# Kernel optimization log

Hardware: AMD Instinct MI355X
Metric: run time of the kernel (lower is better)

Reference implementation:

```python
import jax, jax.numpy as jnp
import numpy as np

N = 32768       # total nodes across the batch of graphs
E = 524288      # total edges
D = 512         # feature dim (dimensions = [512, 512, 512])
G = 512         # number of graphs (64 nodes each)


def setup_inputs() -> dict:
    key = jax.random.key(0)
    ks = jax.random.split(key, 16)
    inp = {
        'feat': jax.random.normal(ks[0], (N, D), jnp.float32),
        'src': jax.random.randint(ks[1], (E,), 0, N, jnp.int32),
        'dst': jax.random.randint(ks[2], (E,), 0, N, jnp.int32),
        'adj_vals': jax.random.uniform(ks[3], (E,), jnp.float32),
        'graph_ids': (jnp.arange(N, dtype=jnp.int32) // (N // G)),
        'W0': jax.random.normal(ks[4], (D, D), jnp.float32) * 0.05,
        'b0': jnp.zeros((D,), jnp.float32),
        'W1': jax.random.normal(ks[5], (D, D), jnp.float32) * 0.05,
        'b1': jnp.zeros((D,), jnp.float32),
        'gW1': jax.random.normal(ks[6], (D, D), jnp.float32) * 0.05,
        'gb1': jnp.zeros((D,), jnp.float32),
        'gW2': jax.random.normal(ks[7], (D, D), jnp.float32) * 0.05,
        'gb2': jnp.zeros((D,), jnp.float32),
        'gW3': jax.random.normal(ks[8], (D, D), jnp.float32) * 0.05,
        'gb3': jnp.zeros((D,), jnp.float32),
        'gWs': jax.random.normal(ks[9], (D, D), jnp.float32) * 0.05,
        'gbs': jnp.zeros((D,), jnp.float32),
    }
    return inp


def reference(feat, src, dst, adj_vals, graph_ids,
              W0, b0, W1, b1,
              gW1, gb1, gW2, gb2, gW3, gb3, gWs, gbs):
    # GCN layer: act(A_hat @ (X W) + b), A_hat given as weighted edge list
    def gcn(h, W, b, act):
        support = h @ W                              # [N, D]
        msg = adj_vals[:, None] * support[src]       # [E, D]
        agg = jax.ops.segment_sum(msg, dst, num_segments=N)
        return act(agg + b)

    h = gcn(feat, W0, b0, jax.nn.relu)               # hidden layer, act=relu
    h = gcn(h, W1, b1, lambda x: x)                  # last layer, identity act

    # pooling: per-graph mean readout -> sigmoid -> repeat-expand back to nodes
    ones = jnp.ones((N, 1), h.dtype)
    counts = jax.ops.segment_sum(ones, graph_ids, num_segments=G)   # [G, 1]
    pooled = jax.ops.segment_sum(h, graph_ids, num_segments=G) / counts
    g = jax.nn.sigmoid(pooled)[graph_ids]            # [N, D] repeat-expanded

    z = jax.nn.relu(g @ gW1 + gb1)
    z = jax.nn.relu(z @ gW2 + gb2)
    z = jax.nn.relu(z @ gW3 + gb3)
    return z + (g @ gWs + gbs)
```

## Files before the change

### kernel.cpp

```cpp
#include <hip/hip_runtime.h>

typedef unsigned int u32;
typedef unsigned short u16;

typedef __attribute__((ext_vector_type(8))) __bf16 bf16x8;
typedef __attribute__((ext_vector_type(4))) float f32x4;
typedef __attribute__((ext_vector_type(2))) float f32x2;
typedef __attribute__((ext_vector_type(4))) u32 u32x4;

#define N_NODES 32768
#define N_EDGES 524288
#define DIM 512
#define N_GRAPHS 512
#define ECAP_ROW 768
#define ECAP 1216
#define ELDS_SZ (ECAP + ECAP / 32 + 1)
#define NB_CONV 8192
#define NB_TR 1536

__device__ __forceinline__ u16 f2b(float f) {
  union { float f; u32 u; } v; v.f = f;
  u32 r = v.u + 0x7FFFu + ((v.u >> 16) & 1u);
  return (u16)(r >> 16);
}
__device__ __forceinline__ u32 pack2(float a, float b) {
  return (u32)f2b(a) | ((u32)f2b(b) << 16);
}
__device__ __forceinline__ float blo(u32 u) { union { u32 u; float f; } v; v.u = u << 16; return v.f; }
__device__ __forceinline__ float bhi(u32 u) { union { u32 u; float f; } v; v.u = u & 0xFFFF0000u; return v.f; }
__device__ __forceinline__ float b2f(u16 u) { union { u32 u; float f; } v; v.u = ((u32)u) << 16; return v.f; }

__device__ __forceinline__ void async16(const void* g, void* l) {
  __builtin_amdgcn_global_load_lds(
      (const __attribute__((address_space(1))) u32*)g,
      (__attribute__((address_space(3))) u32*)l, 16, 0, 0);
}

__device__ __forceinline__ int eidx(int i) { return i + (i >> 5); }

__device__ __forceinline__ void acc8(f32x2* a, u32x4 raw, float v) {
  f32x2 v2 = {v, v};
  a[0] += v2 * f32x2{blo(raw.x), bhi(raw.x)};
  a[1] += v2 * f32x2{blo(raw.y), bhi(raw.y)};
  a[2] += v2 * f32x2{blo(raw.z), bhi(raw.z)};
  a[3] += v2 * f32x2{blo(raw.w), bhi(raw.w)};
}

struct WPack {
  const float* src[6];
  u16* dst[6];
};
__global__ __launch_bounds__(256)
void k_prep(const float* __restrict__ feat, u16* __restrict__ featb, WPack wp,
            const int* __restrict__ dstv, int* __restrict__ counts) {
  __shared__ float tile[32][33];
  const int bid = blockIdx.x, tid = threadIdx.x;
  if (bid < NB_CONV) {
    int i = bid * 256 + tid;
    const float4* p = (const float4*)feat;
    float4 a = p[2 * i], b = p[2 * i + 1];
    uint4 o;
    o.x = pack2(a.x, a.y); o.y = pack2(a.z, a.w);
    o.z = pack2(b.x, b.y); o.w = pack2(b.z, b.w);
    ((uint4*)featb)[i] = o;
  } else if (bid < NB_CONV + NB_TR) {
    int idx = bid - NB_CONV;
    int bz = idx >> 8, rem = idx & 255, by = rem >> 4, bx = rem & 15;
    const float* W = wp.src[bz];
    u16* Wt = wp.dst[bz];
    int tx = tid & 31, ty = tid >> 5;
    int bx32 = bx * 32, by32 = by * 32;
    #pragma unroll
    for (int i = 0; i < 4; i++)
      tile[ty + 8 * i][tx] = W[(size_t)(by32 + ty + 8 * i) * DIM + bx32 + tx];
    __syncthreads();
    #pragma unroll
    for (int i = 0; i < 4; i++)
      Wt[(size_t)(bx32 + ty + 8 * i) * DIM + by32 + tx] = f2b(tile[tx][ty + 8 * i]);
  } else {
    int i = (bid - NB_CONV - NB_TR) * 256 + tid;
    atomicAdd(&counts[dstv[i]], 1);
  }
}

__global__ void k_scan(const int* __restrict__ counts, int* __restrict__ offsets,
                       int* __restrict__ cursor) {
  __shared__ int part[1024];
  int t = threadIdx.x;
  const int4* c4 = (const int4*)counts;
  int4 cv[8];
  #pragma unroll
  for (int j = 0; j < 8; j++) cv[j] = c4[t * 8 + j];
  int loc[32];
  int s = 0;
  #pragma unroll
  for (int j = 0; j < 8; j++) {
    loc[4 * j + 0] = s; s += cv[j].x;
    loc[4 * j + 1] = s; s += cv[j].y;
    loc[4 * j + 2] = s; s += cv[j].z;
    loc[4 * j + 3] = s; s += cv[j].w;
  }
  part[t] = s;
  __syncthreads();
  for (int off = 1; off < 1024; off <<= 1) {
    int v = (t >= off) ? part[t - off] : 0;
    __syncthreads();
    part[t] += v;
    __syncthreads();
  }
  int excl = (t == 0) ? 0 : part[t - 1];
  #pragma unroll
  for (int j = 0; j < 8; j++) {
    int4 o = make_int4(excl + loc[4 * j], excl + loc[4 * j + 1],
                       excl + loc[4 * j + 2], excl + loc[4 * j + 3]);
    ((int4*)offsets)[t * 8 + j] = o;
    ((int4*)cursor)[t * 8 + j] = o;
  }
  if (t == 1023) offsets[N_NODES] = excl + s;
}

__global__ void k_fill(const int* __restrict__ src, const int* __restrict__ dst,
                       const float* __restrict__ vals, int* __restrict__ cursor,
                       int2* __restrict__ epack) {
  int i = blockIdx.x * 256 + threadIdx.x;
  if (i >= N_EDGES) return;
  int d = dst[i];
  int p = atomicAdd(&cursor[d], 1);
  epack[p] = make_int2(src[i] | ((d & 63) << 15), __float_as_int(vals[i]));
}

__global__ __launch_bounds__(256)
void k_gemm_bt(const u16* __restrict__ A, const u16* __restrict__ Bt,
               u16* __restrict__ Cout, int M, int Nout, int K) {
  __shared__ __align__(16) u16 As[128 * 32];
  __shared__ __align__(16) u16 Bs[128 * 32];
  const int tid = threadIdx.x;
  const int l = tid & 63;
  const int w = tid >> 6;
  const int mBase = blockIdx.x * 128;
  const int nBase = blockIdx.y * 128;
  const int wm = (w >> 1) * 64;
  const int wn = (w & 1) * 64;
  const int lrow = l >> 2;
  const int lcol = (l & 3) * 8;
  const int q = l >> 4;
  const int r = l & 15;
  f32x4 acc[4][4] = {};

  for (int k0 = 0; k0 < K; k0 += 32) {
    #pragma unroll
    for (int p = 0; p < 2; p++) {
      int row = w * 32 + p * 16 + lrow;
      async16(A + (size_t)(mBase + row) * K + k0 + lcol, (char*)As + w * 2048 + p * 1024);
      async16(Bt + (size_t)(nBase + row) * K + k0 + lcol, (char*)Bs + w * 2048 + p * 1024);
    }
    __syncthreads();
    bf16x8 af[4], bfr[4];
    #pragma unroll
    for (int i = 0; i < 4; i++) af[i] = *(const bf16x8*)&As[(wm + i * 16 + r) * 32 + q * 8];
    #pragma unroll
    for (int j = 0; j < 4; j++) bfr[j] = *(const bf16x8*)&Bs[(wn + j * 16 + r) * 32 + q * 8];
    #pragma unroll
    for (int i = 0; i < 4; i++)
      #pragma unroll
      for (int j = 0; j < 4; j++)
        acc[i][j] = __builtin_amdgcn_mfma_f32_16x16x32_bf16(af[i], bfr[j], acc[i][j], 0, 0, 0);
    __syncthreads();
  }

  #pragma unroll
  for (int i = 0; i < 4; i++) {
    #pragma unroll
    for (int j = 0; j < 4; j++) {
      int col = nBase + wn + j * 16 + r;
      #pragma unroll
      for (int reg = 0; reg < 4; reg++) {
        int rowg = mBase + wm + i * 16 + q * 4 + reg;
        Cout[(size_t)rowg * Nout + col] = f2b(acc[i][j][reg]);
      }
    }
  }
}

template <bool RELU, bool ADDEND, bool OUTF32, bool SIGMOID>
__global__ __launch_bounds__(256)
void k_gemm_small(const u16* __restrict__ A, const u16* __restrict__ Bt,
                  const float* __restrict__ bias, const u16* __restrict__ addend,
                  void* __restrict__ Cout) {
  constexpr int K = 512, Nout = 512, LDP = 520;
  __shared__ __align__(16) u16 As[64 * LDP];
  __shared__ __align__(16) u16 Bs[64 * LDP];
  const int tid = threadIdx.x;
  const int l = tid & 63;
  const int w = tid >> 6;
  const int mBase = blockIdx.x * 64;
  const int nBase = blockIdx.y * 64;
  const int wm = (w >> 1) * 32;
  const int wn = (w & 1) * 32;
  const int q = l >> 4;
  const int r = l & 15;

  {
    const int row0 = tid >> 6;
    const int c8 = (tid & 63) * 8;
    #pragma unroll
    for (int s = 0; s < 16; s++) {
      int row = s * 4 + row0;
      *(bf16x8*)&As[row * LDP + c8] = *(const bf16x8*)&A[(size_t)(mBase + row) * K + c8];
      *(bf16x8*)&Bs[row * LDP + c8] = *(const bf16x8*)&Bt[(size_t)(nBase + row) * K + c8];
    }
  }
  __syncthreads();

  f32x4 acc[2][2] = {};
  #pragma unroll
  for (int k = 0; k < 16; k++) {
    bf16x8 af0 = *(const bf16x8*)&As[(wm + r) * LDP + k * 32 + q * 8];
    bf16x8 af1 = *(const bf16x8*)&As[(wm + 16 + r) * LDP + k * 32 + q * 8];
    bf16x8 bf0 = *(const bf16x8*)&Bs[(wn + r) * LDP + k * 32 + q * 8];
    bf16x8 bf1 = *(const bf16x8*)&Bs[(wn + 16 + r) * LDP + k * 32 + q * 8];
    acc[0][0] = __builtin_amdgcn_mfma_f32_16x16x32_bf16(af0, bf0, acc[0][0], 0, 0, 0);
    acc[0][1] = __builtin_amdgcn_mfma_f32_16x16x32_bf16(af0, bf1, acc[0][1], 0, 0, 0);
    acc[1][0] = __builtin_amdgcn_mfma_f32_16x16x32_bf16(af1, bf0, acc[1][0], 0, 0, 0);
    acc[1][1] = __builtin_amdgcn_mfma_f32_16x16x32_bf16(af1, bf1, acc[1][1], 0, 0, 0);
  }

  #pragma unroll
  for (int i = 0; i < 2; i++) {
    #pragma unroll
    for (int j = 0; j < 2; j++) {
      int col = nBase + wn + j * 16 + r;
      float bv = bias[col];
      #pragma unroll
      for (int reg = 0; reg < 4; reg++) {
        int rowg = mBase + wm + i * 16 + q * 4 + reg;
        float v = acc[i][j][reg] + bv;
        if (ADDEND) v += b2f(addend[(size_t)rowg * Nout + col]);
        if (RELU) v = fmaxf(v, 0.0f);
        if (SIGMOID) v = 1.0f / (1.0f + expf(-v));
        if (OUTF32) ((float*)Cout)[(size_t)rowg * Nout + col] = v;
        else ((u16*)Cout)[(size_t)rowg * Nout + col] = f2b(v);
      }
    }
  }
}

__global__ __launch_bounds__(256)
void k_agg_row(const u16* __restrict__ support, const int* __restrict__ offsets,
               const int2* __restrict__ epack, const float* __restrict__ bias,
               u16* __restrict__ outp) {
  __shared__ int2 eLds[ECAP_ROW];
  __shared__ unsigned char permLds[32];
  const int tid = threadIdx.x;
  const int chunk = blockIdx.x & 7;
  const int gidx  = blockIdx.x >> 3;
  const int rowBase = gidx * 32;
  const int e0b = offsets[rowBase];
  const int nb = offsets[rowBase + 32] - e0b;
  const bool fits = (nb <= ECAP_ROW);

  if (tid < 32) {
    int deg = offsets[rowBase + tid + 1] - offsets[rowBase + tid];
    u32 key = ((u32)deg << 8) | (u32)tid;
    #pragma unroll
    for (int k = 2; k <= 32; k <<= 1) {
      #pragma unroll
      for (int j = k >> 1; j >= 1; j >>= 1) {
        u32 o = __shfl_xor(key, j);
        bool lower = (tid & j) == 0;
        bool asc = (tid & k) == 0;
        key = ((key < o) == (lower == asc)) ? key : o;
      }
    }
    permLds[tid] = (unsigned char)(key & 255u);
  }
  if (fits) {
    for (int i = tid; i < nb; i += 256) eLds[i] = epack[e0b + i];
  }
  __syncthreads();

  const int wi = tid >> 6;
  const int l  = tid & 63;
  const int grp = l >> 3;
  const int li  = l & 7;
  const int colOff = chunk * 64 + li * 8;
  const u16* spc = support + colOff;

  const int rl = permLds[wi * 8 + grp];
  const int r = rowBase + rl;
  const int re0 = offsets[r] - e0b;
  const int deg = offsets[r + 1] - e0b - re0;

  f32x2 a[4];
  {
    const float4* bp = (const float4*)(bias + colOff);
    float4 x = bp[0], y = bp[1];
    a[0] = f32x2{x.x, x.y}; a[1] = f32x2{x.z, x.w};
    a[2] = f32x2{y.x, y.y}; a[3] = f32x2{y.z, y.w};
  }

  if (fits) {
    int i = 0;
    for (; i + 8 <= deg; i += 8) {
      int2 p[8];
      #pragma unroll
      for (int j = 0; j < 8; j++) p[j] = eLds[re0 + i + j];
      u32x4 rw[8];
      #pragma unroll
      for (int j = 0; j < 8; j++)
        rw[j] = *(const u32x4*)(spc + (size_t)(p[j].x & 32767) * DIM);
      #pragma unroll
      for (int j = 0; j < 8; j++) acc8(a, rw[j], __int_as_float(p[j].y));
    }
    for (; i < deg; i++) {
      int2 p = eLds[re0 + i];
      u32x4 rw = *(const u32x4*)(spc + (size_t)(p.x & 32767) * DIM);
      acc8(a, rw, __int_as_float(p.y));
    }
  } else {
    for (int i = 0; i < deg; i++) {
      int2 p = epack[e0b + re0 + i];
      u32x4 rw = *(const u32x4*)(spc + (size_t)(p.x & 32767) * DIM);
      acc8(a, rw, __int_as_float(p.y));
    }
  }

  #pragma unroll
  for (int i = 0; i < 4; i++) {
    a[i].x = fmaxf(a[i].x, 0.0f);
    a[i].y = fmaxf(a[i].y, 0.0f);
  }
  u32x4 o;
  o.x = pack2(a[0].x, a[0].y); o.y = pack2(a[1].x, a[1].y);
  o.z = pack2(a[2].x, a[2].y); o.w = pack2(a[3].x, a[3].y);
  *(u32x4*)(outp + (size_t)r * DIM + colOff) = o;
}

__global__ __launch_bounds__(256)
void k_agg_pool(const u16* __restrict__ support, const int* __restrict__ offsets,
                const int2* __restrict__ epack, u16* __restrict__ outp) {
  __shared__ int2 eLds[ELDS_SZ];
  __shared__ float redLds[256];

  const int tid = threadIdx.x;
  const int chunk = blockIdx.x & 7;
  const int cidx = blockIdx.x >> 3;
  const int rowBase = cidx * 64;
  const int e0b = offsets[rowBase];
  const int nb = offsets[rowBase + 64] - e0b;
  const bool fits = (nb <= ECAP);

  if (fits) {
    for (int i = tid; i < nb; i += 256) eLds[eidx(i)] = epack[e0b + i];
  }
  __syncthreads();

  const int slot = tid >> 3;
  const int li = tid & 7;
  const int colOff = chunk * 64 + li * 8;
  const u16* spc = support + colOff;
  const int e0 = (nb * slot) >> 5;
  const int e1 = (nb * (slot + 1)) >> 5;

  f32x2 psum[4] = {};

  auto consume = [&](int2 p, u32x4 rw) {
    float v = __int_as_float(p.y);
    f32x2 v2 = {v, v};
    psum[0] += v2 * f32x2{blo(rw.x), bhi(rw.x)};
    psum[1] += v2 * f32x2{blo(rw.y), bhi(rw.y)};
    psum[2] += v2 * f32x2{blo(rw.z), bhi(rw.z)};
    psum[3] += v2 * f32x2{blo(rw.w), bhi(rw.w)};
  };

  if (fits) {
    int i = e0;
    for (; i + 8 <= e1; i += 8) {
      int2 p[8];
      #pragma unroll
      for (int j = 0; j < 8; j++) p[j] = eLds[eidx(i + j)];
      u32x4 rw[8];
      #pragma unroll
      for (int j = 0; j < 8; j++)
        rw[j] = *(const u32x4*)(spc + (size_t)(p[j].x & 32767) * DIM);
      #pragma unroll
      for (int j = 0; j < 8; j++) consume(p[j], rw[j]);
    }
    for (; i < e1; i++) {
      int2 p = eLds[eidx(i)];
      u32x4 rw = *(const u32x4*)(spc + (size_t)(p.x & 32767) * DIM);
      consume(p, rw);
    }
  } else {
    for (int i = e0; i < e1; i++) {
      int2 p = epack[e0b + i];
      u32x4 rw = *(const u32x4*)(spc + (size_t)(p.x & 32767) * DIM);
      consume(p, rw);
    }
  }

  #pragma unroll
  for (int k = 0; k < 4; k++) {
    psum[k].x += __shfl_xor(psum[k].x, 8);  psum[k].y += __shfl_xor(psum[k].y, 8);
    psum[k].x += __shfl_xor(psum[k].x, 16); psum[k].y += __shfl_xor(psum[k].y, 16);
    psum[k].x += __shfl_xor(psum[k].x, 32); psum[k].y += __shfl_xor(psum[k].y, 32);
  }
  const int wi = tid >> 6;
  if (((tid >> 3) & 7) == 0) {
    #pragma unroll
    for (int k = 0; k < 4; k++) {
      redLds[wi * 64 + li * 8 + 2 * k]     = psum[k].x;
      redLds[wi * 64 + li * 8 + 2 * k + 1] = psum[k].y;
    }
  }
  __syncthreads();
  if (tid < 64) {
    float s = redLds[tid] + redLds[64 + tid] + redLds[128 + tid] + redLds[192 + tid];
    outp[(size_t)cidx * DIM + chunk * 64 + tid] = f2b(s * (1.0f / 64.0f));
  }
}

__global__ void k_expand(const float* __restrict__ small, float* __restrict__ out) {
  int i = blockIdx.x * 256 + threadIdx.x;
  int col4 = i & 127;
  int node = i >> 7;
  float4 v = ((const float4*)small)[((node >> 6) << 7) + col4];
  ((float4*)out)[i] = v;
}

extern "C" void kernel_launch(void* const* d_in, const int* in_sizes, int n_in,
                              void* d_out, int out_size, void* d_ws, size_t ws_size,
                              hipStream_t stream) {
  const float* feat = (const float*)d_in[0];
  const int* src    = (const int*)d_in[1];
  const int* dst    = (const int*)d_in[2];
  const float* adj  = (const float*)d_in[3];
  const float* W0  = (const float*)d_in[5];
  const float* b0  = (const float*)d_in[6];
  const float* W1  = (const float*)d_in[7];
  const float* b1  = (const float*)d_in[8];
  const float* gW1 = (const float*)d_in[9];
  const float* gb1 = (const float*)d_in[10];
  const float* gW2 = (const float*)d_in[11];
  const float* gb2 = (const float*)d_in[12];
  const float* gW3 = (const float*)d_in[13];
  const float* gb3 = (const float*)d_in[14];
  const float* gWs = (const float*)d_in[15];
  const float* gbs = (const float*)d_in[16];

  char* ws = (char*)d_ws;
  size_t off = 0;
  auto alloc = [&](size_t bytes) -> void* {
    void* p = ws + off;
    off = (off + bytes + 255) & ~(size_t)255;
    return p;
  };
  u16* bufA = (u16*)alloc((size_t)N_NODES * DIM * 2);
  u16* bufB = (u16*)alloc((size_t)N_NODES * DIM * 2);
  u16* wt[6];
  for (int i = 0; i < 6; i++) wt[i] = (u16*)alloc((size_t)DIM * DIM * 2);
  int* counts   = (int*)alloc((size_t)N_NODES * 4);
  int* offsets  = (int*)alloc((size_t)(N_NODES + 1) * 4);
  int* cursor   = (int*)alloc((size_t)N_NODES * 4);
  int2* epack   = (int2*)alloc((size_t)N_EDGES * 8);
  u16* qb       = (u16*)alloc((size_t)N_GRAPHS * DIM * 2);
  u16* gfeat    = (u16*)alloc((size_t)N_GRAPHS * DIM * 2);
  u16* z1       = (u16*)alloc((size_t)N_GRAPHS * DIM * 2);
  u16* z2       = (u16*)alloc((size_t)N_GRAPHS * DIM * 2);
  u16* z3       = (u16*)alloc((size_t)N_GRAPHS * DIM * 2);
  float* osmall = (float*)alloc((size_t)N_GRAPHS * DIM * 4);

  (void)hipMemsetAsync(counts, 0, (size_t)N_NODES * 4, stream);

  WPack wp;
  wp.src[0] = W0; wp.src[1] = W1; wp.src[2] = gW1; wp.src[3] = gW2; wp.src[4] = gW3; wp.src[5] = gWs;
  for (int i = 0; i < 6; i++) wp.dst[i] = wt[i];

  k_prep<<<NB_CONV + NB_TR + N_EDGES / 256, 256, 0, stream>>>(feat, bufA, wp, dst, counts);
  k_scan<<<1, 1024, 0, stream>>>(counts, offsets, cursor);
  k_fill<<<N_EDGES / 256, 256, 0, stream>>>(src, dst, adj, cursor, epack);

  k_gemm_bt<<<dim3(N_NODES / 128, DIM / 128), 256, 0, stream>>>(bufA, wt[0], bufB, N_NODES, DIM, DIM);
  k_agg_row<<<8192, 256, 0, stream>>>(bufB, offsets, epack, b0, bufA);
  k_agg_pool<<<4096, 256, 0, stream>>>(bufA, offsets, epack, qb);
  k_gemm_small<false, false, false, true><<<dim3(8, 8), 256, 0, stream>>>(qb, wt[1], b1, nullptr, gfeat);

  k_gemm_small<true, false, false, false><<<dim3(8, 8), 256, 0, stream>>>(gfeat, wt[2], gb1, nullptr, z1);
  k_gemm_small<true, false, false, false><<<dim3(8, 8), 256, 0, stream>>>(z1, wt[3], gb2, nullptr, z2);
  k_gemm_small<true, false, false, false><<<dim3(8, 8), 256, 0, stream>>>(z2, wt[4], gb3, nullptr, z3);
  k_gemm_small<false, true, true, false><<<dim3(8, 8), 256, 0, stream>>>(gfeat, wt[5], gbs, z3, osmall);

  k_expand<<<(N_NODES * DIM / 4) / 256, 256, 0, stream>>>(osmall, (float*)d_out);
}
```

Baseline: 371.6 us.

## Fuse edge fill into first GEMM and chain small FF GEMMs with grid barrier

Merges the edge-bucketing fill kernel into the first feature GEMM launch as extra blocks, so the two independent pieces of work run concurrently in one dispatch. It also replaces five back-to-back small GEMM launches with one persistent 64-block kernel that uses a software global barrier between stages. The goal is to cut launch overhead and tail idle time. The cost is reliance on all 64 blocks being co-resident for the spin barrier, plus barrier spin latency.

```diff
diff --git a/kernel.cpp b/kernel.cpp
--- a/kernel.cpp
+++ b/kernel.cpp
@@ -44,6 +44,18 @@
   a[1] += v2 * f32x2{blo(raw.y), bhi(raw.y)};
   a[2] += v2 * f32x2{blo(raw.z), bhi(raw.z)};
   a[3] += v2 * f32x2{blo(raw.w), bhi(raw.w)};
+}
+
+__device__ __forceinline__ void gbar(int* bar, int target) {
+  __syncthreads();
+  if (threadIdx.x == 0) {
+    __threadfence();
+    __hip_atomic_fetch_add(bar, 1, __ATOMIC_RELEASE, __HIP_MEMORY_SCOPE_AGENT);
+    while (__hip_atomic_load(bar, __ATOMIC_ACQUIRE, __HIP_MEMORY_SCOPE_AGENT) < target) {
+      __builtin_amdgcn_s_sleep(2);
+    }
+  }
+  __syncthreads();
 }
 
 struct WPack {
@@ -119,26 +131,27 @@
   if (t == 1023) offsets[N_NODES] = excl + s;
 }
 
-__global__ void k_fill(const int* __restrict__ src, const int* __restrict__ dst,
-                       const float* __restrict__ vals, int* __restrict__ cursor,
-                       int2* __restrict__ epack) {
-  int i = blockIdx.x * 256 + threadIdx.x;
-  if (i >= N_EDGES) return;
-  int d = dst[i];
-  int p = atomicAdd(&cursor[d], 1);
-  epack[p] = make_int2(src[i] | ((d & 63) << 15), __float_as_int(vals[i]));
-}
-
 __global__ __launch_bounds__(256)
-void k_gemm_bt(const u16* __restrict__ A, const u16* __restrict__ Bt,
-               u16* __restrict__ Cout, int M, int Nout, int K) {
+void k_fillgemm(const u16* __restrict__ A, const u16* __restrict__ Bt,
+                u16* __restrict__ Cout,
+                const int* __restrict__ src, const int* __restrict__ dst,
+                const float* __restrict__ vals, int* __restrict__ cursor,
+                int2* __restrict__ epack) {
   __shared__ __align__(16) u16 As[128 * 32];
   __shared__ __align__(16) u16 Bs[128 * 32];
+  if (blockIdx.x >= 1024) {
+    int i = (blockIdx.x - 1024) * 256 + threadIdx.x;
+    int d = dst[i];
+    int p = atomicAdd(&cursor[d], 1);
+    epack[p] = make_int2(src[i] | ((d & 63) << 15), __float_as_int(vals[i]));
+    return;
+  }
+  constexpr int K = DIM, Nout = DIM;
   const int tid = threadIdx.x;
   const int l = tid & 63;
   const int w = tid >> 6;
-  const int mBase = blockIdx.x * 128;
-  const int nBase = blockIdx.y * 128;
+  const int mBase = (blockIdx.x >> 2) * 128;
+  const int nBase = (blockIdx.x & 3) * 128;
   const int wm = (w >> 1) * 64;
   const int wn = (w & 1) * 64;
   const int lrow = l >> 2;
@@ -182,19 +195,15 @@
   }
 }
 
-template <bool RELU, bool ADDEND, bool OUTF32, bool SIGMOID>
-__global__ __launch_bounds__(256)
-void k_gemm_small(const u16* __restrict__ A, const u16* __restrict__ Bt,
-                  const float* __restrict__ bias, const u16* __restrict__ addend,
-                  void* __restrict__ Cout) {
+template <int MODE>
+__device__ __forceinline__ void ff_stage(u16* As, u16* Bs,
+    const u16* __restrict__ A, const u16* __restrict__ Bt,
+    const float* __restrict__ bias, const u16* __restrict__ addend,
+    void* __restrict__ Cout, int mBase, int nBase) {
   constexpr int K = 512, Nout = 512, LDP = 520;
-  __shared__ __align__(16) u16 As[64 * LDP];
-  __shared__ __align__(16) u16 Bs[64 * LDP];
   const int tid = threadIdx.x;
   const int l = tid & 63;
   const int w = tid >> 6;
-  const int mBase = blockIdx.x * 64;
-  const int nBase = blockIdx.y * 64;
   const int wm = (w >> 1) * 32;
   const int wn = (w & 1) * 32;
   const int q = l >> 4;
@@ -235,14 +244,40 @@
       for (int reg = 0; reg < 4; reg++) {
         int rowg = mBase + wm + i * 16 + q * 4 + reg;
         float v = acc[i][j][reg] + bv;
-        if (ADDEND) v += b2f(addend[(size_t)rowg * Nout + col]);
-        if (RELU) v = fmaxf(v, 0.0f);
-        if (SIGMOID) v = 1.0f / (1.0f + expf(-v));
-        if (OUTF32) ((float*)Cout)[(size_t)rowg * Nout + col] = v;
+        if (MODE == 2) v += b2f(addend[(size_t)rowg * Nout + col]);
+        if (MODE == 1) v = fmaxf(v, 0.0f);
+        if (MODE == 0) v = 1.0f / (1.0f + expf(-v));
+        if (MODE == 2) ((float*)Cout)[(size_t)rowg * Nout + col] = v;
         else ((u16*)Cout)[(size_t)rowg * Nout + col] = f2b(v);
       }
     }
   }
+}
+
+__global__ __launch_bounds__(256)
+void k_ffchain(const u16* __restrict__ qb,
+               const u16* __restrict__ w1, const float* __restrict__ b1v,
+               const u16* __restrict__ w2, const float* __restrict__ gb1,
+               const u16* __restrict__ w3, const float* __restrict__ gb2,
+               const u16* __restrict__ w4, const float* __restrict__ gb3,
+               const u16* __restrict__ w5, const float* __restrict__ gbs,
+               u16* __restrict__ gfeat, u16* __restrict__ z1,
+               u16* __restrict__ z2, u16* __restrict__ z3,
+               float* __restrict__ osmall, int* bar) {
+  __shared__ __align__(16) u16 As[64 * 520];
+  __shared__ __align__(16) u16 Bs[64 * 520];
+  const int mBase = (int)(blockIdx.x >> 3) * 64;
+  const int nBase = (int)(blockIdx.x & 7) * 64;
+
+  ff_stage<0>(As, Bs, qb,    w1, b1v, nullptr, gfeat, mBase, nBase);
+  gbar(bar, 64);
+  ff_stage<1>(As, Bs, gfeat, w2, gb1, nullptr, z1, mBase, nBase);
+  gbar(bar, 128);
+  ff_stage<1>(As, Bs, z1,    w3, gb2, nullptr, z2, mBase, nBase);
+  gbar(bar, 192);
+  ff_stage<1>(As, Bs, z2,    w4, gb3, nullptr, z3, mBase, nBase);
+  gbar(bar, 256);
+  ff_stage<2>(As, Bs, gfeat, w5, gbs, z3, osmall, mBase, nBase);
 }
 
 __global__ __launch_bounds__(256)
@@ -469,8 +504,10 @@
   u16* z2       = (u16*)alloc((size_t)N_GRAPHS * DIM * 2);
   u16* z3       = (u16*)alloc((size_t)N_GRAPHS * DIM * 2);
   float* osmall = (float*)alloc((size_t)N_GRAPHS * DIM * 4);
+  int* bar      = (int*)alloc(256);
 
   (void)hipMemsetAsync(counts, 0, (size_t)N_NODES * 4, stream);
+  (void)hipMemsetAsync(bar, 0, 4, stream);
 
   WPack wp;
   wp.src[0] = W0; wp.src[1] = W1; wp.src[2] = gW1; wp.src[3] = gW2; wp.src[4] = gW3; wp.src[5] = gWs;
@@ -478,17 +515,15 @@
 
   k_prep<<<NB_CONV + NB_TR + N_EDGES / 256, 256, 0, stream>>>(feat, bufA, wp, dst, counts);
   k_scan<<<1, 1024, 0, stream>>>(counts, offsets, cursor);
-  k_fill<<<N_EDGES / 256, 256, 0, stream>>>(src, dst, adj, cursor, epack);
-
-  k_gemm_bt<<<dim3(N_NODES / 128, DIM / 128), 256, 0, stream>>>(bufA, wt[0], bufB, N_NODES, DIM, DIM);
+
+  k_fillgemm<<<3072, 256, 0, stream>>>(bufA, wt[0], bufB, src, dst, adj, cursor, epack);
+
   k_agg_row<<<8192, 256, 0, stream>>>(bufB, offsets, epack, b0, bufA);
   k_agg_pool<<<4096, 256, 0, stream>>>(bufA, offsets, epack, qb);
-  k_gemm_small<false, false, false, true><<<dim3(8, 8), 256, 0, stream>>>(qb, wt[1], b1, nullptr, gfeat);
-
-  k_gemm_small<true, false, false, false><<<dim3(8, 8), 256, 0, stream>>>(gfeat, wt[2], gb1, nullptr, z1);
-  k_gemm_small<true, false, false, false><<<dim3(8, 8), 256, 0, stream>>>(z1, wt[3], gb2, nullptr, z2);
-  k_gemm_small<true, false, false, false><<<dim3(8, 8), 256, 0, stream>>>(z2, wt[4], gb3, nullptr, z3);
-  k_gemm_small<false, true, true, false><<<dim3(8, 8), 256, 0, stream>>>(gfeat, wt[5], gbs, z3, osmall);
+
+  k_ffchain<<<64, 256, 0, stream>>>(qb, wt[1], b1, wt[2], gb1, wt[3], gb2,
+                                    wt[4], gb3, wt[5], gbs,
+                                    gfeat, z1, z2, z3, osmall, bar);
 
   k_expand<<<(N_NODES * DIM / 4) / 256, 256, 0, stream>>>(osmall, (float*)d_out);
 }
```

Measured after the change: 365.4 us. No clear change (-1.7%).
